# Kernel tuning notes

Hardware: AMD Instinct MI355X
Metric: run time of the kernel (lower is better)

## Reference

```python
import jax, jax.numpy as jnp
import numpy as np
import math

B, S, H = 2, 2048, 1024
NH, HD = 16, 64  # num heads, head dim; NH*HD == H


def setup_inputs() -> dict:
    key = jax.random.key(0)
    k1, k2, k3 = jax.random.split(key, 3)
    hidden_states = jax.random.normal(k1, (B, S, H), dtype=jnp.float32)
    # causal multiplicative mask [1,1,S,S], 1.0 where attending is allowed
    mask = jnp.tril(jnp.ones((S, S), dtype=jnp.float32))[None, None]
    W_qkv = jax.random.normal(k2, (H, 3 * H), dtype=jnp.float32) * (1.0 / math.sqrt(H))
    b_qkv = jnp.zeros((3 * H,), dtype=jnp.float32)
    W_out = jax.random.normal(k3, (H, H), dtype=jnp.float32) * (1.0 / math.sqrt(H))
    b_out = jnp.zeros((H,), dtype=jnp.float32)
    return {"hidden_states": hidden_states, "mask": mask, "W_qkv": W_qkv,
            "b_qkv": b_qkv, "W_out": W_out, "b_out": b_out}


def reference(hidden_states, mask, W_qkv, b_qkv, W_out, b_out):
    b, s, h = hidden_states.shape
    # fused QKV projection then split into contiguous thirds (split_tensor_along_last_dim)
    qkv = jnp.einsum('bsh,hd->bsd', hidden_states, W_qkv) + b_qkv
    q, k, v = jnp.split(qkv, 3, axis=-1)
    # [b, s, nh*hd] -> [b, nh, s, hd]
    def to_heads(t):
        return t.reshape(b, s, NH, HD).transpose(0, 2, 1, 3)
    q, k, v = to_heads(q), to_heads(k), to_heads(v)
    q = q / jnp.sqrt(jnp.float32(HD))  # scaling_attention_score=True
    scores = jnp.einsum('bhqd,bhkd->bhqk', q, k)  # [b,nh,s,s]
    # multiplicative mask + large-negative bias trick from standard_attention
    scores = scores * mask - 10000.0 * (1.0 - mask)
    probs = jax.nn.softmax(scores, axis=-1)
    ctx = jnp.einsum('bhqk,bhkd->bhqd', probs, v)
    ctx = ctx.transpose(0, 2, 1, 3).reshape(b, s, h)  # [b, s, nh*hd]
    return jnp.einsum('bsh,hd->bsd', ctx, W_out) + b_out
```

## Files before the change

kernel.cpp:

```cpp
#include <hip/hip_runtime.h>
#include <cstdint>
#include <cstddef>

#define NHEAD 16
#define HDIM 64
#define SEQ 2048
#define BATCH 2
#define HID 1024

typedef __bf16 bf16x8 __attribute__((ext_vector_type(8)));
typedef float f32x4 __attribute__((ext_vector_type(4)));

#define AS1 __attribute__((address_space(1)))
#define AS3 __attribute__((address_space(3)))

__device__ __forceinline__ unsigned short f2bf(float f) {
    union { float f; unsigned u; } v; v.f = f;
    unsigned r = v.u + 0x7fffu + ((v.u >> 16) & 1u);
    return (unsigned short)(r >> 16);
}

__device__ __forceinline__ unsigned cvtpk_bf16(float a, float b) {
    unsigned d;
    asm("v_cvt_pk_bf16_f32 %0, %1, %2" : "=v"(d) : "v"(a), "v"(b));
    return d;
}

__global__ __launch_bounds__(256) void convert_f32_bf16(
    const float* __restrict__ in, unsigned short* __restrict__ out, int n) {
    int i = (blockIdx.x * 256 + threadIdx.x) * 8;
    if (i >= n) return;
    float4 a = *(const float4*)(in + i);
    float4 b = *(const float4*)(in + i + 4);
    uint4 o;
    o.x = (unsigned)f2bf(a.x) | ((unsigned)f2bf(a.y) << 16);
    o.y = (unsigned)f2bf(a.z) | ((unsigned)f2bf(a.w) << 16);
    o.z = (unsigned)f2bf(b.x) | ((unsigned)f2bf(b.y) << 16);
    o.w = (unsigned)f2bf(b.z) | ((unsigned)f2bf(b.w) << 16);
    *(uint4*)(out + i) = o;
}

__global__ __launch_bounds__(256) void transpose_f32_bf16(
    const float* __restrict__ in, unsigned short* __restrict__ out, int R, int C) {
    __shared__ unsigned short T[64][72];
    int t = threadIdx.x;
    int c0 = blockIdx.x * 64, r0 = blockIdx.y * 64;
    for (int p = 0; p < 4; ++p) {
        int idx = (p * 256 + t) * 4;
        int row = idx >> 6, col = idx & 63;
        float4 v = *(const float4*)(in + (size_t)(r0 + row) * C + c0 + col);
        T[row][col + 0] = f2bf(v.x);
        T[row][col + 1] = f2bf(v.y);
        T[row][col + 2] = f2bf(v.z);
        T[row][col + 3] = f2bf(v.w);
    }
    __syncthreads();
    for (int p = 0; p < 4; ++p) {
        int idx = (p * 256 + t) * 4;
        int orow = idx >> 6, ocol = idx & 63;
        ushort4 u;
        u.x = T[ocol + 0][orow];
        u.y = T[ocol + 1][orow];
        u.z = T[ocol + 2][orow];
        u.w = T[ocol + 3][orow];
        *(ushort4*)(out + (size_t)(c0 + orow) * R + r0 + ocol) = u;
    }
}

__global__ __launch_bounds__(512, 2) void gemm_qkv(
    const unsigned short* __restrict__ A, const unsigned short* __restrict__ Bt,
    const float* __restrict__ bias,
    unsigned short* __restrict__ Qb, unsigned short* __restrict__ Kb,
    unsigned short* __restrict__ Vt) {
    __shared__ unsigned short LDSu[81920];
    const int NT = 16;
    int tid = threadIdx.x;
    int wave = tid >> 6, lane = tid & 63, ln = lane & 15, quad = lane >> 4;
    int wm = wave >> 2, wn = wave & 3;
    int fid = blockIdx.y * 12 + blockIdx.x;
    int xcd = fid & 7, jj0 = fid >> 3;
    int by = (xcd & 3) * 4 + jj0 / 6;
    int bx = (xcd >> 2) * 6 + jj0 % 6;
    int m0 = by * 256, n0 = bx * 256;

    int rsub = lane >> 3;
    int gs = (lane & 7) ^ rsub;

    auto stage = [&](int h) {
        if (h >= 4 * NT) return;
        int T = h >> 2, jj = h & 3;
        const unsigned short* src;
        int slot;
        if (jj < 2) {
            slot = (2 * T + jj) % 6;
            src = A + (size_t)(m0 + jj * 128) * 1024 + T * 64;
        } else {
            slot = 6 + (2 * T + (jj - 2)) % 4;
            src = Bt + (size_t)(n0 + (jj - 2) * 128) * 1024 + T * 64;
        }
#pragma unroll
        for (int p = 0; p < 2; ++p) {
            __builtin_amdgcn_global_load_lds(
                (const AS1 void*)(src + (size_t)(p * 64 + wave * 8 + rsub) * 1024 + gs * 8),
                (AS3 void*)&LDSu[slot * 8192 + (p * 8 + wave) * 512], 16, 0, 0);
        }
    };

    f32x4 zero4 = {0.f, 0.f, 0.f, 0.f};
    f32x4 acc[8][4];
#pragma unroll
    for (int i = 0; i < 8; ++i)
#pragma unroll
        for (int k = 0; k < 4; ++k) acc[i][k] = zero4;

    for (int h = 0; h < 6; ++h) stage(h);
    asm volatile("s_waitcnt vmcnt(4)" ::: "memory");
    __builtin_amdgcn_s_barrier();

    for (int t = 0; t < NT; ++t) {
        int myA = (2 * t + wm) % 6;
        int myB = 6 + (2 * t + (wn >> 1)) % 4;
        const unsigned short* as = &LDSu[myA * 8192];
        const unsigned short* bs = &LDSu[myB * 8192];
        int brow = (wn & 1) * 64;
        bf16x8 bfr[4][2];
#pragma unroll
        for (int j = 0; j < 4; ++j) {
            if (j == 0) {
#pragma unroll
                for (int fn = 0; fn < 4; ++fn)
#pragma unroll
                    for (int ks = 0; ks < 2; ++ks)
                        bfr[fn][ks] = *(const bf16x8*)
                            &bs[(brow + fn * 16 + ln) * 64 + (((ks * 4 + quad) ^ (ln & 7)) * 8)];
            }
            bf16x8 af[2][2];
#pragma unroll
            for (int mi = 0; mi < 2; ++mi)
#pragma unroll
                for (int ks = 0; ks < 2; ++ks)
                    af[mi][ks] = *(const bf16x8*)
                        &as[((2 * j + mi) * 16 + ln) * 64 + (((ks * 4 + quad) ^ (ln & 7)) * 8)];
            stage(4 * t + j + 6);
            if (j == 3 && t < NT - 1) {
                if (t == NT - 2) asm volatile("s_waitcnt vmcnt(0)" ::: "memory");
                else             asm volatile("s_waitcnt vmcnt(4)" ::: "memory");
            }
            __builtin_amdgcn_s_barrier();
            asm volatile("s_waitcnt lgkmcnt(0)" ::: "memory");
            __builtin_amdgcn_sched_barrier(0);
            __builtin_amdgcn_s_setprio(1);
#pragma unroll
            for (int mi = 0; mi < 2; ++mi)
#pragma unroll
                for (int fn = 0; fn < 4; ++fn) {
                    acc[2 * j + mi][fn] = __builtin_amdgcn_mfma_f32_16x16x32_bf16(
                        af[mi][0], bfr[fn][0], acc[2 * j + mi][fn], 0, 0, 0);
                    acc[2 * j + mi][fn] = __builtin_amdgcn_mfma_f32_16x16x32_bf16(
                        af[mi][1], bfr[fn][1], acc[2 * j + mi][fn], 0, 0, 0);
                }
            __builtin_amdgcn_s_setprio(0);
            __builtin_amdgcn_s_barrier();
        }
    }

    int nbase = n0 + wn * 64;
#pragma unroll
    for (int fn = 0; fn < 4; ++fn) {
        int gn = nbase + fn * 16 + ln;
        float bv = bias[gn];
        int third = gn >> 10;
        int rem = gn & 1023;
        int h = rem >> 6, d = rem & 63;
        if (third == 2) {
#pragma unroll
            for (int fm = 0; fm < 8; ++fm) {
                int gm = m0 + wm * 128 + fm * 16 + quad * 4;
                int b = gm >> 11, s = gm & 2047;
                size_t bh = (size_t)(b * NHEAD + h);
                ushort4 u;
                u.x = f2bf(acc[fm][fn][0] + bv);
                u.y = f2bf(acc[fm][fn][1] + bv);
                u.z = f2bf(acc[fm][fn][2] + bv);
                u.w = f2bf(acc[fm][fn][3] + bv);
                *(ushort4*)&Vt[(bh * HDIM + d) * SEQ + s] = u;
            }
        } else {
            unsigned short* dst = third == 0 ? Qb : Kb;
            float scale = third == 0 ? 0.1803368801111f : 1.0f;
#pragma unroll
            for (int fm = 0; fm < 8; ++fm) {
#pragma unroll
                for (int r = 0; r < 4; ++r) {
                    int gm = m0 + wm * 128 + fm * 16 + quad * 4 + r;
                    int b = gm >> 11, s = gm & 2047;
                    size_t bh = (size_t)(b * NHEAD + h);
                    dst[(bh * SEQ + s) * HDIM + d] = f2bf((acc[fm][fn][r] + bv) * scale);
                }
            }
        }
    }
}

__global__ __launch_bounds__(256) void gemm_out(
    const unsigned short* __restrict__ A, const unsigned short* __restrict__ Bt,
    const float* __restrict__ bias, float* __restrict__ C) {
    __shared__ unsigned short As[128][32];
    __shared__ unsigned short Bs[128][32];
    int t = threadIdx.x;
    int wave = t >> 6, lane = t & 63, ln = lane & 15, quad = lane >> 4;
    int wm = wave >> 1, wn = wave & 1;
    int fid = blockIdx.y * 8 + blockIdx.x;
    int xcd = fid & 7, jj = fid >> 3;
    int by = xcd * 4 + (jj >> 3);
    int bx = jj & 7;
    int m0 = by * 128, n0 = bx * 128;
    int srow = lane >> 2, scol = (lane & 3) * 8;
    f32x4 zero4 = {0.f, 0.f, 0.f, 0.f};
    f32x4 acc[4][4];
    for (int mi = 0; mi < 4; ++mi)
        for (int ni = 0; ni < 4; ++ni) acc[mi][ni] = zero4;
    for (int kt = 0; kt < 1024; kt += 32) {
        for (int p = 0; p < 2; ++p) {
            int r0 = (wave * 2 + p) * 16 + srow;
            __builtin_amdgcn_global_load_lds(
                (const AS1 void*)(A + (size_t)(m0 + r0) * 1024 + kt + scol),
                (AS3 void*)&As[(wave * 2 + p) * 16][0], 16, 0, 0);
            __builtin_amdgcn_global_load_lds(
                (const AS1 void*)(Bt + (size_t)(n0 + r0) * 1024 + kt + scol),
                (AS3 void*)&Bs[(wave * 2 + p) * 16][0], 16, 0, 0);
        }
        __syncthreads();
        bf16x8 af[4], bfr[4];
        for (int mi = 0; mi < 4; ++mi)
            af[mi] = *(const bf16x8*)&As[wm * 64 + mi * 16 + ln][quad * 8];
        for (int ni = 0; ni < 4; ++ni)
            bfr[ni] = *(const bf16x8*)&Bs[wn * 64 + ni * 16 + ln][quad * 8];
        for (int mi = 0; mi < 4; ++mi)
            for (int ni = 0; ni < 4; ++ni)
                acc[mi][ni] = __builtin_amdgcn_mfma_f32_16x16x32_bf16(
                    af[mi], bfr[ni], acc[mi][ni], 0, 0, 0);
        __syncthreads();
    }
    int nbase = n0 + wn * 64;
    for (int ni = 0; ni < 4; ++ni) {
        int gn = nbase + ni * 16 + ln;
        float bv = bias[gn];
        for (int mi = 0; mi < 4; ++mi) {
            for (int r = 0; r < 4; ++r) {
                int gm = m0 + wm * 64 + mi * 16 + quad * 4 + r;
                C[(size_t)gm * HID + gn] = acc[mi][ni][r] + bv;
            }
        }
    }
}

__global__ __launch_bounds__(256, 2) void flash_attn(
    const unsigned short* __restrict__ Qb, const unsigned short* __restrict__ Kb,
    const unsigned short* __restrict__ Vt, unsigned short* __restrict__ Ctx) {
    __shared__ unsigned short KsB[2][64][64];
    __shared__ unsigned short VsB[2][64][64];
    __shared__ unsigned short Ps[2][4][16][72];
    int tid = threadIdx.x;
    int wave = tid >> 6, lane = tid & 63, ln = lane & 15, quad = lane >> 4;

    int id = blockIdx.y * 16 + blockIdx.x;
    int xcd = id & 7, j = id >> 3;
    int bh = xcd * 4 + (j & 3);
    int r0 = (j >> 2) & 7;
    int bxrole = (j < 32) ? r0 : 15 - r0;
    int qiA = bxrole;
    int qiB = 31 - bxrole;
    int q0A = qiA * 64, q0B = qiB * 64;
    const size_t baseQK = (size_t)bh * SEQ * HDIM;
    const size_t baseV = (size_t)bh * HDIM * SEQ;
    int b = bh >> 4, h = bh & 15;

    int rIn = lane >> 3;
    int gsw = ((lane & 7) ^ rIn) * 8;

    bf16x8 aqA0, aqA1, aqB0, aqB1;
    {
        const unsigned short* qp =
            Qb + baseQK + (size_t)(q0A + wave * 16 + ln) * HDIM + quad * 8;
        aqA0 = *(const bf16x8*)qp;
        aqA1 = *(const bf16x8*)(qp + 32);
        qp = Qb + baseQK + (size_t)(q0B + wave * 16 + ln) * HDIM + quad * 8;
        aqB0 = *(const bf16x8*)qp;
        aqB1 = *(const bf16x8*)(qp + 32);
    }

    auto prefetch = [&](int kj, int bi) {
        const unsigned short* kb = Kb + baseQK + (size_t)kj * 64 * HDIM;
        const unsigned short* vb = Vt + baseV + kj * 64;
        for (int c = wave; c < 8; c += 4) {
            __builtin_amdgcn_global_load_lds(
                (const AS1 void*)(kb + (c * 8 + rIn) * HDIM + gsw),
                (AS3 void*)&KsB[bi][c * 8][0], 16, 0, 0);
            __builtin_amdgcn_global_load_lds(
                (const AS1 void*)(vb + (size_t)(c * 8 + rIn) * SEQ + gsw),
                (AS3 void*)&VsB[bi][c * 8][0], 16, 0, 0);
        }
    };

    f32x4 zero4 = {0.f, 0.f, 0.f, 0.f};
    f32x4 oA[4], oB[4];
    float laccA = 0.f, laccB = 0.f;
    for (int i = 0; i < 4; ++i) { oA[i] = zero4; oB[i] = zero4; }

    auto epilogue = [&](const f32x4* o, float lacc, int q0) {
        float sum = lacc;
        sum += __shfl_xor(sum, 16);
        sum += __shfl_xor(sum, 32);
        float linv = __builtin_amdgcn_rcpf(sum);
        size_t rowb = ((size_t)(b * SEQ + q0 + wave * 16 + ln)) * HID + h * 64;
        for (int ni = 0; ni < 4; ++ni) {
            ushort4 u;
            u.x = f2bf(o[ni][0] * linv);
            u.y = f2bf(o[ni][1] * linv);
            u.z = f2bf(o[ni][2] * linv);
            u.w = f2bf(o[ni][3] * linv);
            *(ushort4*)&Ctx[rowb + ni * 16 + quad * 4] = u;
        }
    };

    prefetch(0, 0);
    for (int t = 0; t <= qiB; ++t) {
        __syncthreads();
        if (t < qiB) prefetch(t + 1, (t + 1) & 1);
        int buf = t & 1;
        bool joint = (t <= qiA);

        bf16x8 akf[2][4];
#pragma unroll
        for (int kk = 0; kk < 2; ++kk)
#pragma unroll
            for (int ni = 0; ni < 4; ++ni)
                akf[kk][ni] = *(const bf16x8*)
                    &KsB[buf][ni * 16 + ln][((kk * 4 + quad) ^ (ln & 7)) * 8];
        f32x4 sA[4], sB[4];
#pragma unroll
        for (int ni = 0; ni < 4; ++ni) { sA[ni] = zero4; sB[ni] = zero4; }
        __builtin_amdgcn_s_setprio(1);
#pragma unroll
        for (int kk = 0; kk < 2; ++kk) {
            bf16x8 bq = kk ? aqB1 : aqB0;
#pragma unroll
            for (int ni = 0; ni < 4; ++ni)
                sB[ni] = __builtin_amdgcn_mfma_f32_16x16x32_bf16(akf[kk][ni], bq, sB[ni], 0, 0, 0);
        }
        if (joint) {
#pragma unroll
            for (int kk = 0; kk < 2; ++kk) {
                bf16x8 bq = kk ? aqA1 : aqA0;
#pragma unroll
                for (int ni = 0; ni < 4; ++ni)
                    sA[ni] = __builtin_amdgcn_mfma_f32_16x16x32_bf16(akf[kk][ni], bq, sA[ni], 0, 0, 0);
            }
        }
        __builtin_amdgcn_s_setprio(0);

        if (t == qiB) {
#pragma unroll
            for (int ni = 0; ni < 4; ++ni)
#pragma unroll
                for (int r = 0; r < 4; ++r)
                    if (ni * 16 + quad * 4 + r > wave * 16 + ln) sB[ni][r] = -1.0e38f;
        }
        if (t == qiA) {
#pragma unroll
            for (int ni = 0; ni < 4; ++ni)
#pragma unroll
                for (int r = 0; r < 4; ++r)
                    if (ni * 16 + quad * 4 + r > wave * 16 + ln) sA[ni][r] = -1.0e38f;
        }

#pragma unroll
        for (int ni = 0; ni < 4; ++ni) {
            float e0 = __builtin_amdgcn_exp2f(sB[ni][0]);
            float e1 = __builtin_amdgcn_exp2f(sB[ni][1]);
            float e2 = __builtin_amdgcn_exp2f(sB[ni][2]);
            float e3 = __builtin_amdgcn_exp2f(sB[ni][3]);
            laccB += (e0 + e1) + (e2 + e3);
            uint2 pw;
            pw.x = cvtpk_bf16(e0, e1);
            pw.y = cvtpk_bf16(e2, e3);
            *(uint2*)&Ps[0][wave][ln][ni * 16 + quad * 4] = pw;
        }
        if (joint) {
#pragma unroll
            for (int ni = 0; ni < 4; ++ni) {
                float e0 = __builtin_amdgcn_exp2f(sA[ni][0]);
                float e1 = __builtin_amdgcn_exp2f(sA[ni][1]);
                float e2 = __builtin_amdgcn_exp2f(sA[ni][2]);
                float e3 = __builtin_amdgcn_exp2f(sA[ni][3]);
                laccA += (e0 + e1) + (e2 + e3);
                uint2 pw;
                pw.x = cvtpk_bf16(e0, e1);
                pw.y = cvtpk_bf16(e2, e3);
                *(uint2*)&Ps[1][wave][ln][ni * 16 + quad * 4] = pw;
            }
        }

        bf16x8 avf[2][4];
#pragma unroll
        for (int kk = 0; kk < 2; ++kk)
#pragma unroll
            for (int ni = 0; ni < 4; ++ni)
                avf[kk][ni] = *(const bf16x8*)
                    &VsB[buf][ni * 16 + ln][((kk * 4 + quad) ^ (ln & 7)) * 8];
        {
            bf16x8 bp0 = *(const bf16x8*)&Ps[0][wave][ln][quad * 8];
            bf16x8 bp1 = *(const bf16x8*)&Ps[0][wave][ln][32 + quad * 8];
            __builtin_amdgcn_s_setprio(1);
#pragma unroll
            for (int ni = 0; ni < 4; ++ni)
                oB[ni] = __builtin_amdgcn_mfma_f32_16x16x32_bf16(avf[0][ni], bp0, oB[ni], 0, 0, 0);
#pragma unroll
            for (int ni = 0; ni < 4; ++ni)
                oB[ni] = __builtin_amdgcn_mfma_f32_16x16x32_bf16(avf[1][ni], bp1, oB[ni], 0, 0, 0);
            __builtin_amdgcn_s_setprio(0);
        }
        if (joint) {
            bf16x8 bp0 = *(const bf16x8*)&Ps[1][wave][ln][quad * 8];
            bf16x8 bp1 = *(const bf16x8*)&Ps[1][wave][ln][32 + quad * 8];
            __builtin_amdgcn_s_setprio(1);
#pragma unroll
            for (int ni = 0; ni < 4; ++ni)
                oA[ni] = __builtin_amdgcn_mfma_f32_16x16x32_bf16(avf[0][ni], bp0, oA[ni], 0, 0, 0);
#pragma unroll
            for (int ni = 0; ni < 4; ++ni)
                oA[ni] = __builtin_amdgcn_mfma_f32_16x16x32_bf16(avf[1][ni], bp1, oA[ni], 0, 0, 0);
            __builtin_amdgcn_s_setprio(0);
        }

        if (t == qiA) epilogue(oA, laccA, q0A);
        if (t == qiB) epilogue(oB, laccB, q0B);
    }
}

extern "C" void kernel_launch(void* const* d_in, const int* in_sizes, int n_in,
                              void* d_out, int out_size, void* d_ws, size_t ws_size,
                              hipStream_t stream) {
    const float* X = (const float*)d_in[0];
    const float* Wqkv = (const float*)d_in[2];
    const float* bqkv = (const float*)d_in[3];
    const float* Wout = (const float*)d_in[4];
    const float* bout = (const float*)d_in[5];
    float* out = (float*)d_out;

    char* ws = (char*)d_ws;
    unsigned short* Xb   = (unsigned short*)(ws + 0);
    unsigned short* W1t  = (unsigned short*)(ws + 8388608);
    unsigned short* W2t  = (unsigned short*)(ws + 14680064);
    unsigned short* Qb   = (unsigned short*)(ws + 16777216);
    unsigned short* Kb   = (unsigned short*)(ws + 25165824);
    unsigned short* Vt   = (unsigned short*)(ws + 33554432);
    unsigned short* Ctx  = (unsigned short*)(ws + 41943040);

    convert_f32_bf16<<<2048, 256, 0, stream>>>(X, Xb, 4194304);
    transpose_f32_bf16<<<dim3(48, 16), 256, 0, stream>>>(Wqkv, W1t, 1024, 3072);
    transpose_f32_bf16<<<dim3(16, 16), 256, 0, stream>>>(Wout, W2t, 1024, 1024);
    gemm_qkv<<<dim3(12, 16), 512, 0, stream>>>(Xb, W1t, bqkv, Qb, Kb, Vt);
    flash_attn<<<dim3(16, 32), 256, 0, stream>>>(Qb, Kb, Vt, Ctx);
    gemm_out<<<dim3(8, 32), 256, 0, stream>>>(Ctx, W2t, bout, out);
}
```

Measured before the change: 197.0 us.

## Keep softmax probabilities in registers for PV MFMA and halve out-proj tile height

In flash attention, the PV product now uses the 16x16x16 bf16 MFMA so the probability fragments computed per lane feed the B operand straight from registers. This removes the LDS write and readback of P (the Ps buffer) and frees shared memory, but needs twice as many smaller MFMAs and more V reads from LDS. Separately, the output projection GEMM tile is reduced from 128x128 to 64x128 with twice the grid, to raise the number of workgroups and improve CU occupancy at the cost of more B-tile reloads.

```diff
diff --git a/kernel.cpp b/kernel.cpp
--- a/kernel.cpp
+++ b/kernel.cpp
@@ -10,6 +10,7 @@
 
 typedef __bf16 bf16x8 __attribute__((ext_vector_type(8)));
 typedef float f32x4 __attribute__((ext_vector_type(4)));
+typedef short s16x4 __attribute__((ext_vector_type(4)));
 
 #define AS1 __attribute__((address_space(1)))
 #define AS3 __attribute__((address_space(3)))
@@ -205,38 +206,38 @@
 __global__ __launch_bounds__(256) void gemm_out(
     const unsigned short* __restrict__ A, const unsigned short* __restrict__ Bt,
     const float* __restrict__ bias, float* __restrict__ C) {
-    __shared__ unsigned short As[128][32];
+    __shared__ unsigned short As[64][32];
     __shared__ unsigned short Bs[128][32];
     int t = threadIdx.x;
     int wave = t >> 6, lane = t & 63, ln = lane & 15, quad = lane >> 4;
     int wm = wave >> 1, wn = wave & 1;
     int fid = blockIdx.y * 8 + blockIdx.x;
     int xcd = fid & 7, jj = fid >> 3;
-    int by = xcd * 4 + (jj >> 3);
+    int by = xcd * 8 + (jj >> 3);
     int bx = jj & 7;
-    int m0 = by * 128, n0 = bx * 128;
+    int m0 = by * 64, n0 = bx * 128;
     int srow = lane >> 2, scol = (lane & 3) * 8;
     f32x4 zero4 = {0.f, 0.f, 0.f, 0.f};
-    f32x4 acc[4][4];
-    for (int mi = 0; mi < 4; ++mi)
+    f32x4 acc[2][4];
+    for (int mi = 0; mi < 2; ++mi)
         for (int ni = 0; ni < 4; ++ni) acc[mi][ni] = zero4;
     for (int kt = 0; kt < 1024; kt += 32) {
+        __builtin_amdgcn_global_load_lds(
+            (const AS1 void*)(A + (size_t)(m0 + wave * 16 + srow) * 1024 + kt + scol),
+            (AS3 void*)&As[wave * 16][0], 16, 0, 0);
         for (int p = 0; p < 2; ++p) {
             int r0 = (wave * 2 + p) * 16 + srow;
             __builtin_amdgcn_global_load_lds(
-                (const AS1 void*)(A + (size_t)(m0 + r0) * 1024 + kt + scol),
-                (AS3 void*)&As[(wave * 2 + p) * 16][0], 16, 0, 0);
-            __builtin_amdgcn_global_load_lds(
                 (const AS1 void*)(Bt + (size_t)(n0 + r0) * 1024 + kt + scol),
                 (AS3 void*)&Bs[(wave * 2 + p) * 16][0], 16, 0, 0);
         }
         __syncthreads();
-        bf16x8 af[4], bfr[4];
-        for (int mi = 0; mi < 4; ++mi)
-            af[mi] = *(const bf16x8*)&As[wm * 64 + mi * 16 + ln][quad * 8];
+        bf16x8 af[2], bfr[4];
+        for (int mi = 0; mi < 2; ++mi)
+            af[mi] = *(const bf16x8*)&As[wm * 32 + mi * 16 + ln][quad * 8];
         for (int ni = 0; ni < 4; ++ni)
             bfr[ni] = *(const bf16x8*)&Bs[wn * 64 + ni * 16 + ln][quad * 8];
-        for (int mi = 0; mi < 4; ++mi)
+        for (int mi = 0; mi < 2; ++mi)
             for (int ni = 0; ni < 4; ++ni)
                 acc[mi][ni] = __builtin_amdgcn_mfma_f32_16x16x32_bf16(
                     af[mi], bfr[ni], acc[mi][ni], 0, 0, 0);
@@ -246,9 +247,9 @@
     for (int ni = 0; ni < 4; ++ni) {
         int gn = nbase + ni * 16 + ln;
         float bv = bias[gn];
-        for (int mi = 0; mi < 4; ++mi) {
+        for (int mi = 0; mi < 2; ++mi) {
             for (int r = 0; r < 4; ++r) {
-                int gm = m0 + wm * 64 + mi * 16 + quad * 4 + r;
+                int gm = m0 + wm * 32 + mi * 16 + quad * 4 + r;
                 C[(size_t)gm * HID + gn] = acc[mi][ni][r] + bv;
             }
         }
@@ -260,7 +261,9 @@
     const unsigned short* __restrict__ Vt, unsigned short* __restrict__ Ctx) {
     __shared__ unsigned short KsB[2][64][64];
     __shared__ unsigned short VsB[2][64][64];
+#if !__has_builtin(__builtin_amdgcn_mfma_f32_16x16x16bf16_1k)
     __shared__ unsigned short Ps[2][4][16][72];
+#endif
     int tid = threadIdx.x;
     int wave = tid >> 6, lane = tid & 63, ln = lane & 15, quad = lane >> 4;
 
@@ -375,6 +378,48 @@
                     if (ni * 16 + quad * 4 + r > wave * 16 + ln) sA[ni][r] = -1.0e38f;
         }
 
+#if __has_builtin(__builtin_amdgcn_mfma_f32_16x16x16bf16_1k)
+        s16x4 pbB[4], pbA[4];
+#pragma unroll
+        for (int ni = 0; ni < 4; ++ni) {
+            float e0 = __builtin_amdgcn_exp2f(sB[ni][0]);
+            float e1 = __builtin_amdgcn_exp2f(sB[ni][1]);
+            float e2 = __builtin_amdgcn_exp2f(sB[ni][2]);
+            float e3 = __builtin_amdgcn_exp2f(sB[ni][3]);
+            laccB += (e0 + e1) + (e2 + e3);
+            uint2 pw;
+            pw.x = cvtpk_bf16(e0, e1);
+            pw.y = cvtpk_bf16(e2, e3);
+            pbB[ni] = __builtin_bit_cast(s16x4, pw);
+        }
+        if (joint) {
+#pragma unroll
+            for (int ni = 0; ni < 4; ++ni) {
+                float e0 = __builtin_amdgcn_exp2f(sA[ni][0]);
+                float e1 = __builtin_amdgcn_exp2f(sA[ni][1]);
+                float e2 = __builtin_amdgcn_exp2f(sA[ni][2]);
+                float e3 = __builtin_amdgcn_exp2f(sA[ni][3]);
+                laccA += (e0 + e1) + (e2 + e3);
+                uint2 pw;
+                pw.x = cvtpk_bf16(e0, e1);
+                pw.y = cvtpk_bf16(e2, e3);
+                pbA[ni] = __builtin_bit_cast(s16x4, pw);
+            }
+        }
+        __builtin_amdgcn_s_setprio(1);
+#pragma unroll
+        for (int ni = 0; ni < 4; ++ni) {
+#pragma unroll
+            for (int db = 0; db < 4; ++db) {
+                s16x4 av = *(const s16x4*)&VsB[buf][db * 16 + ln]
+                    [(((ni * 2 + (quad >> 1)) ^ (ln & 7)) * 8) + (quad & 1) * 4];
+                oB[db] = __builtin_amdgcn_mfma_f32_16x16x16bf16_1k(av, pbB[ni], oB[db], 0, 0, 0);
+                if (joint)
+                    oA[db] = __builtin_amdgcn_mfma_f32_16x16x16bf16_1k(av, pbA[ni], oA[db], 0, 0, 0);
+            }
+        }
+        __builtin_amdgcn_s_setprio(0);
+#else
 #pragma unroll
         for (int ni = 0; ni < 4; ++ni) {
             float e0 = __builtin_amdgcn_exp2f(sB[ni][0]);
@@ -401,7 +446,6 @@
                 *(uint2*)&Ps[1][wave][ln][ni * 16 + quad * 4] = pw;
             }
         }
-
         bf16x8 avf[2][4];
 #pragma unroll
         for (int kk = 0; kk < 2; ++kk)
@@ -433,6 +477,7 @@
                 oA[ni] = __builtin_amdgcn_mfma_f32_16x16x32_bf16(avf[1][ni], bp1, oA[ni], 0, 0, 0);
             __builtin_amdgcn_s_setprio(0);
         }
+#endif
 
         if (t == qiA) epilogue(oA, laccA, q0A);
         if (t == qiB) epilogue(oB, laccB, q0B);
@@ -463,5 +508,5 @@
     transpose_f32_bf16<<<dim3(16, 16), 256, 0, stream>>>(Wout, W2t, 1024, 1024);
     gemm_qkv<<<dim3(12, 16), 512, 0, stream>>>(Xb, W1t, bqkv, Qb, Kb, Vt);
     flash_attn<<<dim3(16, 32), 256, 0, stream>>>(Qb, Kb, Vt, Ctx);
-    gemm_out<<<dim3(8, 32), 256, 0, stream>>>(Ctx, W2t, bout, out);
-}
+    gemm_out<<<dim3(8, 64), 256, 0, stream>>>(Ctx, W2t, bout, out);
+}
```

Result: slower. 208.3 us (+5.7%).
